# Kernel optimization log

Measured on AMD Instinct MI355X. Metric: run time of the kernel, lower is better.

The kernel has to match this reference:

```python
import jax, jax.numpy as jnp
import numpy as np

HEAD_DIM = 128


def setup_inputs() -> dict:
    key = jax.random.key(0)
    k1, k2, k3 = jax.random.split(key, 3)
    B, S, H, HKV, D = 2, 2048, 32, 8, HEAD_DIM
    q = jax.random.normal(k1, (B, S, H, D), dtype=jnp.float32)
    k = jax.random.normal(k2, (B, S, HKV, D), dtype=jnp.float32)
    v = jax.random.normal(k3, (B, S, HKV, D), dtype=jnp.float32)
    return {"q": q, "k": k, "v": v}


def reference(q, k, v):
    # Grouped-query causal attention.
    # q: [B,S,H,D], k/v: [B,S,Hkv,D], H = Hkv * G
    B, S, H, D = q.shape
    Hkv = k.shape[2]
    G = H // Hkv
    scaling = D ** (-0.5)
    qg = q.reshape(B, S, Hkv, G, D)
    # scores: [B, Hkv, G, S_q, S_k]
    scores = jnp.einsum('bskgd,btkd->bkgst', qg, k) * scaling
    causal = jnp.tril(jnp.ones((S, S), dtype=bool))
    scores = jnp.where(causal, scores, jnp.finfo(scores.dtype).min)
    probs = jax.nn.softmax(scores, axis=-1)
    out = jnp.einsum('bkgst,btkd->bskgd', probs, v)
    return out.reshape(B, S, H, D)
```

## Files before the change

kernel.cpp:

```cpp
#include <hip/hip_runtime.h>
#include <hip/hip_bf16.h>

#define BB 2
#define SS 2048
#define NH 32
#define NKV 8
#define GQ (NH / NKV)
#define DD 128
#define QBLK 128
#define KVBLK 64
#define NQT (SS / QBLK)
#define NTHREADS 512

#define KPAD (DD + 8)
#define VPAD (KVBLK + 8)

typedef __bf16 bf16x8 __attribute__((ext_vector_type(8)));
typedef short short8 __attribute__((ext_vector_type(8)));
typedef float f32x4 __attribute__((ext_vector_type(4)));
typedef unsigned int u32x4 __attribute__((ext_vector_type(4)));
typedef unsigned short u16x4 __attribute__((ext_vector_type(4)));

__device__ inline bf16x8 cvt_bf16x8(float4 a, float4 b) {
  bf16x8 r;
  r[0] = (__bf16)a.x; r[1] = (__bf16)a.y; r[2] = (__bf16)a.z; r[3] = (__bf16)a.w;
  r[4] = (__bf16)b.x; r[5] = (__bf16)b.y; r[6] = (__bf16)b.z; r[7] = (__bf16)b.w;
  return r;
}

__global__ __launch_bounds__(NTHREADS, 2)
void attn_mfma_v2(const float* __restrict__ qp, const float* __restrict__ kp,
                  const float* __restrict__ vp, float* __restrict__ op)
{
  __shared__ __align__(16) short kpl[KVBLK][KPAD];
  __shared__ __align__(16) short vtp[DD][VPAD];
  __shared__ __align__(16) short ppl[8][16][VPAD];

  const int tid  = threadIdx.x;
  const int wave = tid >> 6;
  const int lane = tid & 63;
  const int lhi  = lane >> 4;
  const int llo  = lane & 15;

  const int bid = blockIdx.x;
  const int bh  = bid % (BB * NH);
  const int qt  = NQT - 1 - bid / (BB * NH);
  const int b   = bh / NH;
  const int h   = bh % NH;
  const int kh  = h / GQ;

  const int q0 = qt * QBLK;
  const int qw = q0 + wave * 16;

  const float scale = 0.08838834764831845f;

  bf16x8 qf[4];
  {
    const float* qrow = qp + (((size_t)b * SS + (qw + llo)) * NH + h) * DD;
    #pragma unroll
    for (int kc = 0; kc < 4; ++kc) {
      const int d0 = kc * 32 + lhi * 8;
      float4 a = *(const float4*)(qrow + d0);
      float4 c = *(const float4*)(qrow + d0 + 4);
      a.x *= scale; a.y *= scale; a.z *= scale; a.w *= scale;
      c.x *= scale; c.y *= scale; c.z *= scale; c.w *= scale;
      qf[kc] = cvt_bf16x8(a, c);
    }
  }

  f32x4 oacc[8];
  #pragma unroll
  for (int f = 0; f < 8; ++f) oacc[f] = (f32x4){0.f, 0.f, 0.f, 0.f};
  float m_i = -1e30f, l_i = 0.f;

  const int ntiles = q0 / KVBLK + 2;

  for (int t = 0; t < ntiles; ++t) {
    const int t0 = t * KVBLK;
    __syncthreads();

    #pragma unroll
    for (int it = 0; it < 2; ++it) {
      const int c   = tid + it * NTHREADS;
      const int row = c >> 4, c16 = c & 15;
      const float* src = kp + (((size_t)b * SS + (t0 + row)) * NKV + kh) * DD + c16 * 8;
      float4 a = *(const float4*)src;
      float4 d = *(const float4*)(src + 4);
      *(u32x4*)&kpl[row][c16 * 8] = __builtin_bit_cast(u32x4, cvt_bf16x8(a, d));
    }
    #pragma unroll
    for (int it = 0; it < 2; ++it) {
      const int c  = tid + it * NTHREADS;
      const int dv = c & 127, t8 = c >> 7;
      const float* src = vp + (((size_t)b * SS + (t0 + t8 * 8)) * NKV + kh) * DD + dv;
      bf16x8 e;
      #pragma unroll
      for (int i = 0; i < 8; ++i)
        e[i] = (__bf16)src[(size_t)i * (NKV * DD)];
      *(u32x4*)&vtp[dv][t8 * 8] = __builtin_bit_cast(u32x4, e);
    }
    __syncthreads();

    if (t0 > qw + 15) continue;

    f32x4 sfrag[4];
    #pragma unroll
    for (int cc = 0; cc < 4; ++cc) {
      f32x4 acc = (f32x4){0.f, 0.f, 0.f, 0.f};
      const int r = cc * 16 + llo;
      #pragma unroll
      for (int kc = 0; kc < 4; ++kc) {
        u32x4 kb = *(const u32x4*)&kpl[r][(kc * 4 + lhi) * 8];
        acc = __builtin_amdgcn_mfma_f32_16x16x32_bf16(
                  __builtin_bit_cast(bf16x8, kb), qf[kc], acc, 0, 0, 0);
      }
      sfrag[cc] = acc;
    }

    if (t0 + KVBLK - 1 > qw) {
      const int qg = qw + llo;
      #pragma unroll
      for (int cc = 0; cc < 4; ++cc)
        #pragma unroll
        for (int j = 0; j < 4; ++j) {
          const int tg = t0 + cc * 16 + lhi * 4 + j;
          if (tg > qg) sfrag[cc][j] = -1e30f;
        }
    }

    float tmx = sfrag[0][0];
    #pragma unroll
    for (int cc = 0; cc < 4; ++cc)
      #pragma unroll
      for (int j = 0; j < 4; ++j)
        tmx = fmaxf(tmx, sfrag[cc][j]);
    tmx = fmaxf(tmx, __shfl_xor(tmx, 16));
    tmx = fmaxf(tmx, __shfl_xor(tmx, 32));
    const float mnew = fmaxf(m_i, tmx);
    const float corr = __expf(m_i - mnew);
    m_i = mnew;
    float s = 0.f;
    #pragma unroll
    for (int cc = 0; cc < 4; ++cc)
      #pragma unroll
      for (int j = 0; j < 4; ++j) {
        const float p = __expf(sfrag[cc][j] - mnew);
        sfrag[cc][j] = p;
        s += p;
      }
    s += __shfl_xor(s, 16);
    s += __shfl_xor(s, 32);
    l_i = l_i * corr + s;

    #pragma unroll
    for (int j = 0; j < 4; ++j) {
      const float cj = __shfl(corr, lhi * 4 + j);
      #pragma unroll
      for (int f = 0; f < 8; ++f) oacc[f][j] *= cj;
    }

    #pragma unroll
    for (int cc = 0; cc < 4; ++cc) {
      u16x4 pk;
      pk[0] = __builtin_bit_cast(unsigned short, (__bf16)sfrag[cc][0]);
      pk[1] = __builtin_bit_cast(unsigned short, (__bf16)sfrag[cc][1]);
      pk[2] = __builtin_bit_cast(unsigned short, (__bf16)sfrag[cc][2]);
      pk[3] = __builtin_bit_cast(unsigned short, (__bf16)sfrag[cc][3]);
      *(u16x4*)&ppl[wave][llo][cc * 16 + lhi * 4] = pk;
    }

    asm volatile("s_waitcnt lgkmcnt(0)" ::: "memory");
    __builtin_amdgcn_sched_barrier(0);

    #pragma unroll
    for (int kc2 = 0; kc2 < 2; ++kc2) {
      u32x4 pa = *(const u32x4*)&ppl[wave][llo][(kc2 * 4 + lhi) * 8];
      #pragma unroll
      for (int f = 0; f < 8; ++f) {
        u32x4 vb = *(const u32x4*)&vtp[f * 16 + llo][(kc2 * 4 + lhi) * 8];
        oacc[f] = __builtin_amdgcn_mfma_f32_16x16x32_bf16(
                      __builtin_bit_cast(bf16x8, pa),
                      __builtin_bit_cast(bf16x8, vb), oacc[f], 0, 0, 0);
      }
    }
  }

  #pragma unroll
  for (int j = 0; j < 4; ++j) {
    const float lj = __shfl(l_i, lhi * 4 + j);
    const float inv = 1.f / lj;
    const int qg = qw + lhi * 4 + j;
    float* orow = op + (((size_t)b * SS + qg) * NH + h) * DD;
    #pragma unroll
    for (int f = 0; f < 8; ++f)
      orow[f * 16 + llo] = oacc[f][j] * inv;
  }
}

extern "C" void kernel_launch(void* const* d_in, const int* in_sizes, int n_in,
                              void* d_out, int out_size, void* d_ws, size_t ws_size,
                              hipStream_t stream) {
  const float* q = (const float*)d_in[0];
  const float* k = (const float*)d_in[1];
  const float* v = (const float*)d_in[2];
  float* out = (float*)d_out;
  dim3 grid(BB * NH * NQT);
  dim3 block(NTHREADS);
  attn_mfma_v2<<<grid, block, 0, stream>>>(q, k, v, out);
}
```

Before: 146.1 us.

## Give each wave 32 query rows with 4 waves per block

The block shrinks from 8 waves to 4, and each wave now handles two 16-row query sub-tiles. Each K and V fragment read from LDS therefore feeds two MFMAs instead of one, halving LDS read traffic per unit of compute. In exchange, register pressure roughly doubles for accumulators and Q fragments, and each thread does twice as many global-to-LDS conversion loads per tile. Causal skipping also becomes coarser, at 32-row granularity.

```diff
diff --git a/kernel.cpp b/kernel.cpp
--- a/kernel.cpp
+++ b/kernel.cpp
@@ -10,7 +10,8 @@
 #define QBLK 128
 #define KVBLK 64
 #define NQT (SS / QBLK)
-#define NTHREADS 512
+#define NTHREADS 256
+#define NWAVES 4
 
 #define KPAD (DD + 8)
 #define VPAD (KVBLK + 8)
@@ -29,12 +30,12 @@
 }
 
 __global__ __launch_bounds__(NTHREADS, 2)
-void attn_mfma_v2(const float* __restrict__ qp, const float* __restrict__ kp,
-                  const float* __restrict__ vp, float* __restrict__ op)
+void attn_mfma_w32(const float* __restrict__ qp, const float* __restrict__ kp,
+                   const float* __restrict__ vp, float* __restrict__ op)
 {
   __shared__ __align__(16) short kpl[KVBLK][KPAD];
   __shared__ __align__(16) short vtp[DD][VPAD];
-  __shared__ __align__(16) short ppl[8][16][VPAD];
+  __shared__ __align__(16) short ppl[NWAVES][32][VPAD];
 
   const int tid  = threadIdx.x;
   const int wave = tid >> 6;
@@ -50,13 +51,14 @@
   const int kh  = h / GQ;
 
   const int q0 = qt * QBLK;
-  const int qw = q0 + wave * 16;
+  const int qw = q0 + wave * 32;
 
   const float scale = 0.08838834764831845f;
 
-  bf16x8 qf[4];
-  {
-    const float* qrow = qp + (((size_t)b * SS + (qw + llo)) * NH + h) * DD;
+  bf16x8 qf[2][4];
+  #pragma unroll
+  for (int u = 0; u < 2; ++u) {
+    const float* qrow = qp + (((size_t)b * SS + (qw + u * 16 + llo)) * NH + h) * DD;
     #pragma unroll
     for (int kc = 0; kc < 4; ++kc) {
       const int d0 = kc * 32 + lhi * 8;
@@ -64,14 +66,16 @@
       float4 c = *(const float4*)(qrow + d0 + 4);
       a.x *= scale; a.y *= scale; a.z *= scale; a.w *= scale;
       c.x *= scale; c.y *= scale; c.z *= scale; c.w *= scale;
-      qf[kc] = cvt_bf16x8(a, c);
+      qf[u][kc] = cvt_bf16x8(a, c);
     }
   }
 
-  f32x4 oacc[8];
+  f32x4 oacc[2][8];
   #pragma unroll
-  for (int f = 0; f < 8; ++f) oacc[f] = (f32x4){0.f, 0.f, 0.f, 0.f};
-  float m_i = -1e30f, l_i = 0.f;
+  for (int u = 0; u < 2; ++u)
+    #pragma unroll
+    for (int f = 0; f < 8; ++f) oacc[u][f] = (f32x4){0.f, 0.f, 0.f, 0.f};
+  float m_i[2] = {-1e30f, -1e30f}, l_i[2] = {0.f, 0.f};
 
   const int ntiles = q0 / KVBLK + 2;
 
@@ -80,7 +84,7 @@
     __syncthreads();
 
     #pragma unroll
-    for (int it = 0; it < 2; ++it) {
+    for (int it = 0; it < 4; ++it) {
       const int c   = tid + it * NTHREADS;
       const int row = c >> 4, c16 = c & 15;
       const float* src = kp + (((size_t)b * SS + (t0 + row)) * NKV + kh) * DD + c16 * 8;
@@ -89,7 +93,7 @@
       *(u32x4*)&kpl[row][c16 * 8] = __builtin_bit_cast(u32x4, cvt_bf16x8(a, d));
     }
     #pragma unroll
-    for (int it = 0; it < 2; ++it) {
+    for (int it = 0; it < 4; ++it) {
       const int c  = tid + it * NTHREADS;
       const int dv = c & 127, t8 = c >> 7;
       const float* src = vp + (((size_t)b * SS + (t0 + t8 * 8)) * NKV + kh) * DD + dv;
@@ -101,72 +105,80 @@
     }
     __syncthreads();
 
-    if (t0 > qw + 15) continue;
-
-    f32x4 sfrag[4];
+    if (t0 > qw + 31) continue;
+
+    f32x4 sf[2][4];
     #pragma unroll
     for (int cc = 0; cc < 4; ++cc) {
-      f32x4 acc = (f32x4){0.f, 0.f, 0.f, 0.f};
+      f32x4 a0 = (f32x4){0.f, 0.f, 0.f, 0.f};
+      f32x4 a1 = (f32x4){0.f, 0.f, 0.f, 0.f};
       const int r = cc * 16 + llo;
       #pragma unroll
       for (int kc = 0; kc < 4; ++kc) {
         u32x4 kb = *(const u32x4*)&kpl[r][(kc * 4 + lhi) * 8];
-        acc = __builtin_amdgcn_mfma_f32_16x16x32_bf16(
-                  __builtin_bit_cast(bf16x8, kb), qf[kc], acc, 0, 0, 0);
-      }
-      sfrag[cc] = acc;
+        const bf16x8 kf = __builtin_bit_cast(bf16x8, kb);
+        a0 = __builtin_amdgcn_mfma_f32_16x16x32_bf16(kf, qf[0][kc], a0, 0, 0, 0);
+        a1 = __builtin_amdgcn_mfma_f32_16x16x32_bf16(kf, qf[1][kc], a1, 0, 0, 0);
+      }
+      sf[0][cc] = a0; sf[1][cc] = a1;
     }
 
     if (t0 + KVBLK - 1 > qw) {
-      const int qg = qw + llo;
+      #pragma unroll
+      for (int u = 0; u < 2; ++u) {
+        const int qg = qw + u * 16 + llo;
+        #pragma unroll
+        for (int cc = 0; cc < 4; ++cc)
+          #pragma unroll
+          for (int j = 0; j < 4; ++j) {
+            const int tg = t0 + cc * 16 + lhi * 4 + j;
+            if (tg > qg) sf[u][cc][j] = -1e30f;
+          }
+      }
+    }
+
+    #pragma unroll
+    for (int u = 0; u < 2; ++u) {
+      float tmx = sf[u][0][0];
       #pragma unroll
       for (int cc = 0; cc < 4; ++cc)
         #pragma unroll
+        for (int j = 0; j < 4; ++j)
+          tmx = fmaxf(tmx, sf[u][cc][j]);
+      tmx = fmaxf(tmx, __shfl_xor(tmx, 16));
+      tmx = fmaxf(tmx, __shfl_xor(tmx, 32));
+      const float mnew = fmaxf(m_i[u], tmx);
+      const float corr = __expf(m_i[u] - mnew);
+      m_i[u] = mnew;
+      float s = 0.f;
+      #pragma unroll
+      for (int cc = 0; cc < 4; ++cc)
+        #pragma unroll
         for (int j = 0; j < 4; ++j) {
-          const int tg = t0 + cc * 16 + lhi * 4 + j;
-          if (tg > qg) sfrag[cc][j] = -1e30f;
+          const float p = __expf(sf[u][cc][j] - mnew);
+          sf[u][cc][j] = p;
+          s += p;
         }
-    }
-
-    float tmx = sfrag[0][0];
-    #pragma unroll
-    for (int cc = 0; cc < 4; ++cc)
-      #pragma unroll
-      for (int j = 0; j < 4; ++j)
-        tmx = fmaxf(tmx, sfrag[cc][j]);
-    tmx = fmaxf(tmx, __shfl_xor(tmx, 16));
-    tmx = fmaxf(tmx, __shfl_xor(tmx, 32));
-    const float mnew = fmaxf(m_i, tmx);
-    const float corr = __expf(m_i - mnew);
-    m_i = mnew;
-    float s = 0.f;
-    #pragma unroll
-    for (int cc = 0; cc < 4; ++cc)
+      s += __shfl_xor(s, 16);
+      s += __shfl_xor(s, 32);
+      l_i[u] = l_i[u] * corr + s;
+
       #pragma unroll
       for (int j = 0; j < 4; ++j) {
-        const float p = __expf(sfrag[cc][j] - mnew);
-        sfrag[cc][j] = p;
-        s += p;
-      }
-    s += __shfl_xor(s, 16);
-    s += __shfl_xor(s, 32);
-    l_i = l_i * corr + s;
-
-    #pragma unroll
-    for (int j = 0; j < 4; ++j) {
-      const float cj = __shfl(corr, lhi * 4 + j);
-      #pragma unroll
-      for (int f = 0; f < 8; ++f) oacc[f][j] *= cj;
-    }
-
-    #pragma unroll
-    for (int cc = 0; cc < 4; ++cc) {
-      u16x4 pk;
-      pk[0] = __builtin_bit_cast(unsigned short, (__bf16)sfrag[cc][0]);
-      pk[1] = __builtin_bit_cast(unsigned short, (__bf16)sfrag[cc][1]);
-      pk[2] = __builtin_bit_cast(unsigned short, (__bf16)sfrag[cc][2]);
-      pk[3] = __builtin_bit_cast(unsigned short, (__bf16)sfrag[cc][3]);
-      *(u16x4*)&ppl[wave][llo][cc * 16 + lhi * 4] = pk;
+        const float cj = __shfl(corr, lhi * 4 + j);
+        #pragma unroll
+        for (int f = 0; f < 8; ++f) oacc[u][f][j] *= cj;
+      }
+
+      #pragma unroll
+      for (int cc = 0; cc < 4; ++cc) {
+        u16x4 pk;
+        pk[0] = __builtin_bit_cast(unsigned short, (__bf16)sf[u][cc][0]);
+        pk[1] = __builtin_bit_cast(unsigned short, (__bf16)sf[u][cc][1]);
+        pk[2] = __builtin_bit_cast(unsigned short, (__bf16)sf[u][cc][2]);
+        pk[3] = __builtin_bit_cast(unsigned short, (__bf16)sf[u][cc][3]);
+        *(u16x4*)&ppl[wave][u * 16 + llo][cc * 16 + lhi * 4] = pk;
+      }
     }
 
     asm volatile("s_waitcnt lgkmcnt(0)" ::: "memory");
@@ -174,27 +186,32 @@
 
     #pragma unroll
     for (int kc2 = 0; kc2 < 2; ++kc2) {
-      u32x4 pa = *(const u32x4*)&ppl[wave][llo][(kc2 * 4 + lhi) * 8];
+      u32x4 pa0 = *(const u32x4*)&ppl[wave][llo][(kc2 * 4 + lhi) * 8];
+      u32x4 pa1 = *(const u32x4*)&ppl[wave][16 + llo][(kc2 * 4 + lhi) * 8];
       #pragma unroll
       for (int f = 0; f < 8; ++f) {
         u32x4 vb = *(const u32x4*)&vtp[f * 16 + llo][(kc2 * 4 + lhi) * 8];
-        oacc[f] = __builtin_amdgcn_mfma_f32_16x16x32_bf16(
-                      __builtin_bit_cast(bf16x8, pa),
-                      __builtin_bit_cast(bf16x8, vb), oacc[f], 0, 0, 0);
+        const bf16x8 vf = __builtin_bit_cast(bf16x8, vb);
+        oacc[0][f] = __builtin_amdgcn_mfma_f32_16x16x32_bf16(
+                         __builtin_bit_cast(bf16x8, pa0), vf, oacc[0][f], 0, 0, 0);
+        oacc[1][f] = __builtin_amdgcn_mfma_f32_16x16x32_bf16(
+                         __builtin_bit_cast(bf16x8, pa1), vf, oacc[1][f], 0, 0, 0);
       }
     }
   }
 
   #pragma unroll
-  for (int j = 0; j < 4; ++j) {
-    const float lj = __shfl(l_i, lhi * 4 + j);
-    const float inv = 1.f / lj;
-    const int qg = qw + lhi * 4 + j;
-    float* orow = op + (((size_t)b * SS + qg) * NH + h) * DD;
-    #pragma unroll
-    for (int f = 0; f < 8; ++f)
-      orow[f * 16 + llo] = oacc[f][j] * inv;
-  }
+  for (int u = 0; u < 2; ++u)
+    #pragma unroll
+    for (int j = 0; j < 4; ++j) {
+      const float lj = __shfl(l_i[u], lhi * 4 + j);
+      const float inv = 1.f / lj;
+      const int qg = qw + u * 16 + lhi * 4 + j;
+      float* orow = op + (((size_t)b * SS + qg) * NH + h) * DD;
+      #pragma unroll
+      for (int f = 0; f < 8; ++f)
+        orow[f * 16 + llo] = oacc[u][f][j] * inv;
+    }
 }
 
 extern "C" void kernel_launch(void* const* d_in, const int* in_sizes, int n_in,
@@ -206,5 +223,5 @@
   float* out = (float*)d_out;
   dim3 grid(BB * NH * NQT);
   dim3 block(NTHREADS);
-  attn_mfma_v2<<<grid, block, 0, stream>>>(q, k, v, out);
+  attn_mfma_w32<<<grid, block, 0, stream>>>(q, k, v, out);
 }
```

After: 184.7 us. +26.5%, slower.
